# Optimization experiments

Hardware: AMD Instinct MI355X
Metric: run time of the kernel (lower is better)

## Reference

```python
import jax, jax.numpy as jnp
import numpy as np

TAU = 1.0
NUM_CENTROIDS = 8
COMMITMENT_COST = 0.25


def setup_inputs() -> dict:
    key = jax.random.key(0)
    kx, kc = jax.random.split(key)
    B, T, D = 8, 2048, 512
    K = 4096  # codebook_size
    x = jax.random.normal(kx, (B, T, D), dtype=jnp.float32)
    # variance_scaling(1.0, fan_in, uniform): limit = sqrt(3/D)
    limit = np.sqrt(3.0 / D).astype(np.float32)
    codebook = jax.random.uniform(kc, (K, D), dtype=jnp.float32, minval=-limit, maxval=limit)
    return {"x": x, "codebook": codebook}


def _squared_euclidean_distance(a, b):
    # a: [N, D], b: [K, D] -> [N, K]
    a2 = jnp.sum(a * a, axis=-1, keepdims=True)          # [N, 1]
    b2 = jnp.sum(b * b, axis=-1)                          # [K]
    ab = a @ b.T                                          # [N, K]
    return a2 - 2.0 * ab + b2


def reference(x, codebook):
    B, T, D = x.shape
    K = codebook.shape[0]
    flat = x.reshape(-1, D)
    distances = _squared_euclidean_distance(flat, codebook).reshape(B, T, K)
    weights = jax.nn.softmax(-distances / TAU, axis=-1)
    top_weights, top_indices = jax.lax.top_k(weights, NUM_CENTROIDS)  # [B,T,k]
    top_weights = top_weights / jnp.sum(top_weights, axis=-1, keepdims=True)
    # decode_ids: weighted sum of gathered codebook rows (== one-hot einsum)
    gathered = jnp.take(codebook, top_indices, axis=0)                # [B,T,k,D]
    quantized = jnp.einsum('btk,btkd->btd', top_weights, gathered)
    # train=True losses (entropy_loss_ratio == 0 -> skipped)
    e_latent_loss = jnp.mean((jax.lax.stop_gradient(quantized) - x) ** 2) * COMMITMENT_COST
    q_latent_loss = jnp.mean((quantized - jax.lax.stop_gradient(x)) ** 2)
    loss = e_latent_loss.astype(jnp.float32) + q_latent_loss.astype(jnp.float32)
    # straight-through estimator
    quantized = x + jax.lax.stop_gradient(quantized - x)
    return quantized, loss
```

## Files before the change

### kernel.cpp

```cpp
#include <hip/hip_runtime.h>
#include <stdint.h>

#define D_DIM 512
#define K_CB  4096
#define N_TOK 16384
#define TOPK  8

#define TOKB  32
#define TOKE  16
#define NPASS 16
#define NSEL  16

typedef __attribute__((ext_vector_type(4)))  int       i32x4;
typedef __attribute__((ext_vector_type(8)))  int       i32x8;
typedef __attribute__((ext_vector_type(16))) float     f32x16;
typedef __attribute__((ext_vector_type(4)))  float     f32x4;
typedef __attribute__((ext_vector_type(4)))  _Float16  f16x4;
typedef __attribute__((ext_vector_type(8)))  _Float16  f16x8;

template<int N>
__device__ __forceinline__ void inskey(unsigned int k, unsigned int (&ts)[N]) {
    #pragma unroll
    for (int q = 0; q < N; ++q) {
        unsigned int hi = ts[q] > k ? ts[q] : k;
        unsigned int lo = ts[q] > k ? k : ts[q];
        ts[q] = hi; k = lo;
    }
}

__device__ __forceinline__ f32x16 mfma_step(i32x4 al, i32x4 ah, i32x4 bl, i32x4 bh,
                                            f32x16 acc) {
    return __builtin_amdgcn_mfma_scale_f32_32x32x64_f8f6f4(
        __builtin_shufflevector(al, ah, 0,1,2,3,4,5,6,7),
        __builtin_shufflevector(bl, bh, 0,1,2,3,4,5,6,7),
        acc, 0, 0, 0, 0x7F7F7F7F, 0, 0x7F7F7F7F);
}

__global__ __launch_bounds__(256) void conv_cb_kernel(
    const float* __restrict__ cb, unsigned char* __restrict__ cbf8,
    _Float16* __restrict__ cbh, float* __restrict__ cnorm,
    float* __restrict__ loss, unsigned int* __restrict__ ticket) {
    const int t = threadIdx.x, gb = blockIdx.x;
    if (gb == 0 && t == 0) { *loss = 0.f; *ticket = 0u; }
    const int r16 = t >> 4, c = t & 15;
    const int row = gb * 16 + r16;
    const float* src = cb + (size_t)row * D_DIM + c * 32;
    _Float16* hrow = cbh + (size_t)row * D_DIM + c * 32;
    float sq = 0.f;
    unsigned int d[8];
    #pragma unroll
    for (int i = 0; i < 8; ++i) {
        float4 v = ((const float4*)src)[i];
        sq += v.x*v.x + v.y*v.y + v.z*v.z + v.w*v.w;
        int dd = __builtin_amdgcn_cvt_pk_fp8_f32(64.f * v.x, 64.f * v.y, 0, false);
        dd     = __builtin_amdgcn_cvt_pk_fp8_f32(64.f * v.z, 64.f * v.w, dd, true);
        d[i] = (unsigned int)dd;
        f16x4 hv = {(_Float16)v.x, (_Float16)v.y, (_Float16)v.z, (_Float16)v.w};
        *(f16x4*)(hrow + i * 4) = hv;
    }
    sq += __shfl_down(sq, 8, 16);
    sq += __shfl_down(sq, 4, 16);
    sq += __shfl_down(sq, 2, 16);
    sq += __shfl_down(sq, 1, 16);
    if (c == 0) cnorm[row] = sq;
    const int g = row >> 5, row32 = row & 31;
    const int s = c >> 1, khalf = c & 1;
    unsigned char* base = cbf8 + (size_t)g * 16384 + (size_t)s * 2048
                        + (size_t)(khalf * 32 + row32) * 16;
    i32x4 lo = {(int)d[0], (int)d[1], (int)d[2], (int)d[3]};
    i32x4 hi = {(int)d[4], (int)d[5], (int)d[6], (int)d[7]};
    *(i32x4*)(base)        = lo;
    *(i32x4*)(base + 1024) = hi;
}

__global__ __launch_bounds__(512, 4) void vq_main(
    const float* __restrict__ x, const unsigned char* __restrict__ cbf8,
    const float* __restrict__ cnorm, int* __restrict__ tki_g)
{
    __shared__ union {
        struct {
            unsigned char xs8[TOKB * D_DIM];
            float ncn[K_CB];
        } s;
        unsigned int keys[256 * 32];
    } u;
    __shared__ unsigned int pk[TOKB * 65];

    const int t    = threadIdx.x;
    const int lane = t & 63;
    const int w    = t >> 6;
    const int m32  = lane & 31;
    const int half = lane >> 5;
    const int tok0 = blockIdx.x * TOKB;

    const char* cb8l = (const char*)cbf8 + (size_t)lane * 16;

    {
        const int token = t >> 4, c = t & 15;
        const int s2 = c >> 1, lh = c & 1;
        const f32x4* src = (const f32x4*)(x + (size_t)(tok0 + token) * D_DIM + c * 32);
        unsigned int d[8];
        #pragma unroll
        for (int i = 0; i < 8; ++i) {
            f32x4 v = src[i];
            int dd = __builtin_amdgcn_cvt_pk_fp8_f32(16.f * v.x, 16.f * v.y, 0, false);
            dd     = __builtin_amdgcn_cvt_pk_fp8_f32(16.f * v.z, 16.f * v.w, dd, true);
            d[i] = (unsigned int)dd;
        }
        unsigned char* base = u.s.xs8 + s2 * 2048 + (lh * 32 + token) * 16;
        i32x4 lo = {(int)d[0], (int)d[1], (int)d[2], (int)d[3]};
        i32x4 hi = {(int)d[4], (int)d[5], (int)d[6], (int)d[7]};
        *(i32x4*)(base)        = lo;
        *(i32x4*)(base + 1024) = hi;
    }
    {
        float4 v0 = ((const float4*)cnorm)[t];
        float4 v1 = ((const float4*)cnorm)[t + 512];
        float4 n0 = {32768.f - 512.f * v0.x, 32768.f - 512.f * v0.y,
                     32768.f - 512.f * v0.z, 32768.f - 512.f * v0.w};
        float4 n1 = {32768.f - 512.f * v1.x, 32768.f - 512.f * v1.y,
                     32768.f - 512.f * v1.z, 32768.f - 512.f * v1.w};
        *(float4*)&u.s.ncn[t * 4]         = n0;
        *(float4*)&u.s.ncn[(t + 512) * 4] = n1;
    }
    __syncthreads();

    unsigned int tsA[8], tsB[8];
    #pragma unroll
    for (int i = 0; i < 8; ++i) { tsA[i] = 0u; tsB[i] = 0u; }

    const unsigned char* pb = u.s.xs8 + lane * 16;

    for (int pp = 0; pp < NPASS; ++pp) {
        const int p  = (pp + 2 * w) & 15;
        const int ga = p * 8 + w;
        f32x16 acc;
        #pragma unroll
        for (int g = 0; g < 4; ++g) {
            float4 n0 = *(const float4*)&u.s.ncn[ga * 32 + g * 8 + 4 * half];
            acc[g*4+0]=n0.x; acc[g*4+1]=n0.y; acc[g*4+2]=n0.z; acc[g*4+3]=n0.w;
        }
        const char* ab = cb8l + (size_t)ga * 16384;
        #pragma unroll
        for (int s = 0; s < 8; ++s) {
            i32x4 al = *(const i32x4*)(ab + s * 2048);
            i32x4 ah = *(const i32x4*)(ab + s * 2048 + 1024);
            i32x4 bl = *(const i32x4*)(pb + s * 2048);
            i32x4 bh = *(const i32x4*)(pb + s * 2048 + 1024);
            acc = mfma_step(al, ah, bl, bh, acc);
        }
        const unsigned int K0 = 4095u - (unsigned int)(ga * 32) - 4u * (unsigned int)half;
        if ((pp & 1) == 0) {
            #pragma unroll
            for (int r = 0; r < 16; ++r) {
                const unsigned int cr = (unsigned int)((r & 3) + 8 * (r >> 2));
                inskey((__float_as_uint(acc[r]) & 0xFFFFF000u) | (K0 - cr), tsA);
            }
        } else {
            #pragma unroll
            for (int r = 0; r < 16; ++r) {
                const unsigned int cr = (unsigned int)((r & 3) + 8 * (r >> 2));
                inskey((__float_as_uint(acc[r]) & 0xFFFFF000u) | (K0 - cr), tsB);
            }
        }
    }

    __syncthreads();
    {
        const int L0 = w * 4 + half * 2;
        #pragma unroll
        for (int e = 0; e < 8; ++e) {
            u.keys[(L0 * 8 + e) * 32 + m32]       = tsA[e];
            u.keys[((L0 + 1) * 8 + e) * 32 + m32] = tsB[e];
        }
    }
    __syncthreads();
    if (t < 128) {
        const int token = t >> 2, sub = t & 3;
        unsigned int bs[16];
        #pragma unroll
        for (int i = 0; i < 16; ++i) bs[i] = 0u;
        #pragma unroll 2
        for (int k = 0; k < 64; ++k) inskey(u.keys[(sub * 64 + k) * 32 + token], bs);
        #pragma unroll
        for (int e = 0; e < 16; ++e) pk[token * 65 + sub * 16 + e] = bs[e];
    }
    __syncthreads();
    if (t < TOKB) {
        unsigned int bs[NSEL];
        #pragma unroll
        for (int i = 0; i < NSEL; ++i) bs[i] = 0u;
        #pragma unroll 2
        for (int k = 0; k < 64; ++k) inskey(pk[t * 65 + k], bs);
        #pragma unroll
        for (int r = 0; r < NSEL; ++r)
            tki_g[(size_t)blockIdx.x * (TOKB * NSEL) + t * NSEL + r] =
                4095 - (int)(bs[r] & 0xFFFu);
    }
}

__global__ __launch_bounds__(256) void vq_epi(
    const float* __restrict__ x, const _Float16* __restrict__ cbh,
    const float* __restrict__ cnorm, const int* __restrict__ tki_g,
    float* __restrict__ out, float* __restrict__ loss_acc,
    unsigned int* __restrict__ ticket)
{
    __shared__ int   tkl[TOKE * NSEL];
    __shared__ float tks[TOKE * 17];
    __shared__ float tkw[TOKE * TOPK];
    __shared__ int   tkif[TOKE * TOPK];
    __shared__ float redbuf[4];

    const int t    = threadIdx.x;
    const int lane = t & 63;
    const int w    = t >> 6;
    const int tok0 = blockIdx.x * TOKE;

    tkl[t] = tki_g[(size_t)blockIdx.x * (TOKE * NSEL) + t];
    __syncthreads();

    {
        const int token = t >> 4, sl = t & 15;
        const f32x4* xr = (const f32x4*)(x + (size_t)(tok0 + token) * D_DIM);
        f32x4 xv[8];
        #pragma unroll
        for (int i = 0; i < 4; ++i) {
            xv[2*i]   = xr[(sl + 16*i) * 2];
            xv[2*i+1] = xr[(sl + 16*i) * 2 + 1];
        }
        #pragma unroll
        for (int hh = 0; hh < 2; ++hh) {
            float pd[8];
            #pragma unroll
            for (int e = 0; e < 8; ++e) {
                const int idx = tkl[token * NSEL + hh * 8 + e];
                const f16x8* cr = (const f16x8*)(cbh + (size_t)idx * D_DIM);
                float dot = 0.f;
                #pragma unroll
                for (int i = 0; i < 4; ++i) {
                    f16x8 cv = cr[sl + 16*i];
                    dot += xv[2*i].x   * (float)cv[0] + xv[2*i].y   * (float)cv[1]
                         + xv[2*i].z   * (float)cv[2] + xv[2*i].w   * (float)cv[3]
                         + xv[2*i+1].x * (float)cv[4] + xv[2*i+1].y * (float)cv[5]
                         + xv[2*i+1].z * (float)cv[6] + xv[2*i+1].w * (float)cv[7];
                }
                pd[e] = dot;
            }
            #pragma unroll
            for (int e = 0; e < 8; ++e) {
                pd[e] += __shfl_down(pd[e], 8, 16);
                pd[e] += __shfl_down(pd[e], 4, 16);
                pd[e] += __shfl_down(pd[e], 2, 16);
                pd[e] += __shfl_down(pd[e], 1, 16);
            }
            if (sl == 0) {
                #pragma unroll
                for (int e = 0; e < 8; ++e)
                    tks[token * 17 + hh * 8 + e] =
                        2.f * pd[e] - cnorm[tkl[token * NSEL + hh * 8 + e]];
            }
        }
    }
    __syncthreads();
    if (t < TOKE) {
        unsigned int bs[8];
        #pragma unroll
        for (int i = 0; i < 8; ++i) bs[i] = 0u;
        #pragma unroll
        for (int e = 0; e < NSEL; ++e) {
            unsigned int uu = __float_as_uint(tks[t * 17 + e]);
            uu ^= (unsigned int)((int)uu >> 31) | 0x80000000u;
            inskey((uu & 0xFFFFFFF0u) | (unsigned int)e, bs);
        }
        const float m = tks[t * 17 + (int)(bs[0] & 15u)];
        float wv[TOPK], sum = 0.f;
        int ids[TOPK];
        #pragma unroll
        for (int r = 0; r < TOPK; ++r) {
            const int e = (int)(bs[r] & 15u);
            wv[r] = __expf(tks[t * 17 + e] - m); sum += wv[r];
            ids[r] = tkl[t * NSEL + e];
        }
        const float inv = 1.f / sum;
        #pragma unroll
        for (int r = 0; r < TOPK; ++r) {
            tkw[t * TOPK + r] = wv[r] * inv;
            tkif[t * TOPK + r] = ids[r];
        }
    }
    __syncthreads();
    float lsum = 0.f;
    #pragma unroll 1
    for (int it = 0; it < (TOKE * (D_DIM / 4)) / 256; ++it) {
        const int p = it * 256 + t;
        const int token = p >> 7, d4 = p & 127;
        float4 q = {0.f, 0.f, 0.f, 0.f};
        #pragma unroll
        for (int e = 0; e < TOPK; ++e) {
            const float wv = tkw[token * TOPK + e];
            const int  idx = tkif[token * TOPK + e];
            f16x4 cv = *(const f16x4*)(cbh + (size_t)idx * D_DIM + d4 * 4);
            q.x += wv * (float)cv[0]; q.y += wv * (float)cv[1];
            q.z += wv * (float)cv[2]; q.w += wv * (float)cv[3];
        }
        const size_t go = (size_t)(tok0 + token) * (D_DIM / 4) + d4;
        f32x4 xv = __builtin_nontemporal_load((const f32x4*)x + go);
        const float ex = q.x - xv.x, ey = q.y - xv.y, ez = q.z - xv.z, ew = q.w - xv.w;
        lsum += ex*ex + ey*ey + ez*ez + ew*ew;
        f32x4 qv = {q.x, q.y, q.z, q.w};
        __builtin_nontemporal_store(qv, (f32x4*)out + go);
    }
    #pragma unroll
    for (int off = 32; off > 0; off >>= 1) lsum += __shfl_down(lsum, off, 64);
    if (lane == 0) redbuf[w] = lsum;
    __syncthreads();
    if (t == 0) {
        float s = 0.f;
        #pragma unroll
        for (int i = 0; i < 4; ++i) s += redbuf[i];
        atomicAdd(loss_acc, s);
        __threadfence();
        unsigned int prev = atomicAdd(ticket, 1u);
        if (prev == (unsigned int)(gridDim.x - 1)) {
            __threadfence();
            float total = atomicAdd(loss_acc, 0.f);
            out[(size_t)N_TOK * D_DIM] = 1.25f * total / (float)((size_t)N_TOK * D_DIM);
        }
    }
}

extern "C" void kernel_launch(void* const* d_in, const int* in_sizes, int n_in,
                              void* d_out, int out_size, void* d_ws, size_t ws_size,
                              hipStream_t stream) {
    const float* x  = (const float*)d_in[0];
    const float* cb = (const float*)d_in[1];
    float* out = (float*)d_out;

    char* ws = (char*)d_ws;
    unsigned char* cbf8   = (unsigned char*)ws;
    _Float16*      cbh    = (_Float16*)(ws + 2097152);
    float*         cnorm  = (float*)(ws + 6291456);
    float*         loss   = (float*)(ws + 6307840);
    unsigned int*  ticket = (unsigned int*)(ws + 6307904);
    int*           tki_g  = (int*)(ws + 6308096);

    conv_cb_kernel<<<256, 256, 0, stream>>>(cb, cbf8, cbh, cnorm, loss, ticket);
    vq_main<<<N_TOK / TOKB, 512, 0, stream>>>(x, cbf8, cnorm, tki_g);
    vq_epi<<<N_TOK / TOKE, 256, 0, stream>>>(x, cbh, cnorm, tki_g, out, loss, ticket);
}
```

Before: 222.7 us.

## Process two codebook groups per pass and use 32-byte contiguous fp8 fragments

Each wave now computes two 32-column codebook groups per pass with two independent MFMA accumulators, and both reuse the same token operand loaded from LDS. The pass count is halved to match. The fp8 layouts for codebook and tokens now keep each lane's 32-byte K fragment contiguous, so one 256-bit load replaces two 128-bit loads plus a shuffle. This cuts LDS reads of the token operand and gives two independent MFMA chains for more instruction-level parallelism, at the cost of more registers under the 512-thread, 4-block launch bound.

```diff
diff --git a/kernel.cpp b/kernel.cpp
--- a/kernel.cpp
+++ b/kernel.cpp
@@ -8,7 +8,7 @@
 
 #define TOKB  32
 #define TOKE  16
-#define NPASS 16
+#define NPASS 8
 #define NSEL  16
 
 typedef __attribute__((ext_vector_type(4)))  int       i32x4;
@@ -28,12 +28,9 @@
     }
 }
 
-__device__ __forceinline__ f32x16 mfma_step(i32x4 al, i32x4 ah, i32x4 bl, i32x4 bh,
-                                            f32x16 acc) {
+__device__ __forceinline__ f32x16 mfma8(i32x8 a, i32x8 b, f32x16 acc) {
     return __builtin_amdgcn_mfma_scale_f32_32x32x64_f8f6f4(
-        __builtin_shufflevector(al, ah, 0,1,2,3,4,5,6,7),
-        __builtin_shufflevector(bl, bh, 0,1,2,3,4,5,6,7),
-        acc, 0, 0, 0, 0x7F7F7F7F, 0, 0x7F7F7F7F);
+        a, b, acc, 0, 0, 0, 0x7F7F7F7F, 0, 0x7F7F7F7F);
 }
 
 __global__ __launch_bounds__(256) void conv_cb_kernel(
@@ -64,20 +61,20 @@
     sq += __shfl_down(sq, 1, 16);
     if (c == 0) cnorm[row] = sq;
     const int g = row >> 5, row32 = row & 31;
-    const int s = c >> 1, khalf = c & 1;
+    const int s = c >> 1, kh = c & 1;
     unsigned char* base = cbf8 + (size_t)g * 16384 + (size_t)s * 2048
-                        + (size_t)(khalf * 32 + row32) * 16;
+                        + (size_t)(kh * 32 + row32) * 32;
     i32x4 lo = {(int)d[0], (int)d[1], (int)d[2], (int)d[3]};
     i32x4 hi = {(int)d[4], (int)d[5], (int)d[6], (int)d[7]};
-    *(i32x4*)(base)        = lo;
-    *(i32x4*)(base + 1024) = hi;
+    *(i32x4*)(base)      = lo;
+    *(i32x4*)(base + 16) = hi;
 }
 
 __global__ __launch_bounds__(512, 4) void vq_main(
     const float* __restrict__ x, const unsigned char* __restrict__ cbf8,
     const float* __restrict__ cnorm, int* __restrict__ tki_g)
 {
-    __shared__ union {
+    __shared__ __align__(32) union {
         struct {
             unsigned char xs8[TOKB * D_DIM];
             float ncn[K_CB];
@@ -93,7 +90,7 @@
     const int half = lane >> 5;
     const int tok0 = blockIdx.x * TOKB;
 
-    const char* cb8l = (const char*)cbf8 + (size_t)lane * 16;
+    const char* cb8l = (const char*)cbf8 + (size_t)lane * 32;
 
     {
         const int token = t >> 4, c = t & 15;
@@ -107,11 +104,11 @@
             dd     = __builtin_amdgcn_cvt_pk_fp8_f32(16.f * v.z, 16.f * v.w, dd, true);
             d[i] = (unsigned int)dd;
         }
-        unsigned char* base = u.s.xs8 + s2 * 2048 + (lh * 32 + token) * 16;
+        unsigned char* base = u.s.xs8 + s2 * 2048 + (lh * 32 + token) * 32;
         i32x4 lo = {(int)d[0], (int)d[1], (int)d[2], (int)d[3]};
         i32x4 hi = {(int)d[4], (int)d[5], (int)d[6], (int)d[7]};
-        *(i32x4*)(base)        = lo;
-        *(i32x4*)(base + 1024) = hi;
+        *(i32x4*)(base)      = lo;
+        *(i32x4*)(base + 16) = hi;
     }
     {
         float4 v0 = ((const float4*)cnorm)[t];
@@ -129,39 +126,35 @@
     #pragma unroll
     for (int i = 0; i < 8; ++i) { tsA[i] = 0u; tsB[i] = 0u; }
 
-    const unsigned char* pb = u.s.xs8 + lane * 16;
+    const unsigned char* pb = u.s.xs8 + lane * 32;
 
     for (int pp = 0; pp < NPASS; ++pp) {
-        const int p  = (pp + 2 * w) & 15;
-        const int ga = p * 8 + w;
-        f32x16 acc;
+        const int q   = (pp + w) & 7;
+        const int ga0 = q * 16 + w;
+        f32x16 acc0, acc1;
         #pragma unroll
         for (int g = 0; g < 4; ++g) {
-            float4 n0 = *(const float4*)&u.s.ncn[ga * 32 + g * 8 + 4 * half];
-            acc[g*4+0]=n0.x; acc[g*4+1]=n0.y; acc[g*4+2]=n0.z; acc[g*4+3]=n0.w;
-        }
-        const char* ab = cb8l + (size_t)ga * 16384;
+            float4 n0 = *(const float4*)&u.s.ncn[ga0 * 32 + g * 8 + 4 * half];
+            float4 n1 = *(const float4*)&u.s.ncn[(ga0 + 8) * 32 + g * 8 + 4 * half];
+            acc0[g*4+0]=n0.x; acc0[g*4+1]=n0.y; acc0[g*4+2]=n0.z; acc0[g*4+3]=n0.w;
+            acc1[g*4+0]=n1.x; acc1[g*4+1]=n1.y; acc1[g*4+2]=n1.z; acc1[g*4+3]=n1.w;
+        }
+        const char* ab0 = cb8l + (size_t)ga0 * 16384;
         #pragma unroll
         for (int s = 0; s < 8; ++s) {
-            i32x4 al = *(const i32x4*)(ab + s * 2048);
-            i32x4 ah = *(const i32x4*)(ab + s * 2048 + 1024);
-            i32x4 bl = *(const i32x4*)(pb + s * 2048);
-            i32x4 bh = *(const i32x4*)(pb + s * 2048 + 1024);
-            acc = mfma_step(al, ah, bl, bh, acc);
-        }
-        const unsigned int K0 = 4095u - (unsigned int)(ga * 32) - 4u * (unsigned int)half;
-        if ((pp & 1) == 0) {
-            #pragma unroll
-            for (int r = 0; r < 16; ++r) {
-                const unsigned int cr = (unsigned int)((r & 3) + 8 * (r >> 2));
-                inskey((__float_as_uint(acc[r]) & 0xFFFFF000u) | (K0 - cr), tsA);
-            }
-        } else {
-            #pragma unroll
-            for (int r = 0; r < 16; ++r) {
-                const unsigned int cr = (unsigned int)((r & 3) + 8 * (r >> 2));
-                inskey((__float_as_uint(acc[r]) & 0xFFFFF000u) | (K0 - cr), tsB);
-            }
+            i32x8 a0 = *(const i32x8*)(ab0 + s * 2048);
+            i32x8 a1 = *(const i32x8*)(ab0 + 131072 + s * 2048);
+            i32x8 b  = *(const i32x8*)(pb + s * 2048);
+            acc0 = mfma8(a0, b, acc0);
+            acc1 = mfma8(a1, b, acc1);
+        }
+        const unsigned int K0a = 4095u - (unsigned int)(ga0 * 32) - 4u * (unsigned int)half;
+        const unsigned int K0b = K0a - 256u;
+        #pragma unroll
+        for (int r = 0; r < 16; ++r) {
+            const unsigned int cr = (unsigned int)((r & 3) + 8 * (r >> 2));
+            inskey((__float_as_uint(acc0[r]) & 0xFFFFF000u) | (K0a - cr), tsA);
+            inskey((__float_as_uint(acc1[r]) & 0xFFFFF000u) | (K0b - cr), tsB);
         }
     }
 
```

Measured after the change: 277.5 us. 24.6% more time.
